# Kernel tuning notes

Measured on AMD Instinct MI355X. Metric: run time of the kernel, lower is better.

The kernel has to match this reference:

```python
import jax, jax.numpy as jnp
from jax import lax
import numpy as np

B, T, H, V, C = 64, 64, 1024, 32000, 10
Z, CD = 32, 8  # latent dim, cond embedding dim


def lstm_scan(x_tbh, h0, c0, Wih, Whh, bih, bhh):
    """PyTorch-convention LSTM over time. x_tbh: [T,B,H]; returns hs [T,B,H]."""
    def step(carry, x):
        h, c = carry
        gates = x @ Wih.T + bih + h @ Whh.T + bhh  # [B,4H]
        i, f, g, o = jnp.split(gates, 4, axis=-1)
        c = jax.nn.sigmoid(f) * c + jax.nn.sigmoid(i) * jnp.tanh(g)
        h = jax.nn.sigmoid(o) * jnp.tanh(c)
        return (h, c), h
    _, hs = lax.scan(step, (h0, c0), x_tbh)
    return hs


def setup_inputs() -> dict:
    key = jax.random.key(0)
    ks = jax.random.split(key, 24)
    s = 0.02
    d = {
        'input_word': jax.random.randint(ks[0], (B, T), 0, V),
        'cond': jax.random.randint(ks[1], (B,), 0, C),
        'emb_N': jax.random.normal(ks[2], (V, H), jnp.float32) * s,
        'Wih_N': jax.random.normal(ks[3], (4 * H, H), jnp.float32) * s,
        'Whh_N': jax.random.normal(ks[4], (4 * H, H), jnp.float32) * s,
        'bih_N': jnp.zeros((4 * H,), jnp.float32),
        'bhh_N': jnp.zeros((4 * H,), jnp.float32),
        'emb_D': jax.random.normal(ks[5], (V, H), jnp.float32) * s,
        'Wih_D': jax.random.normal(ks[6], (4 * H, H), jnp.float32) * s,
        'Whh_D': jax.random.normal(ks[7], (4 * H, H), jnp.float32) * s,
        'bih_D': jnp.zeros((4 * H,), jnp.float32),
        'bhh_D': jnp.zeros((4 * H,), jnp.float32),
        'emb_cond': jax.random.normal(ks[8], (C, CD), jnp.float32) * s,
        'W_mean': jax.random.normal(ks[9], (Z, H), jnp.float32) * s,
        'b_mean': jnp.zeros((Z,), jnp.float32),
        'W_logvar': jax.random.normal(ks[10], (Z, H), jnp.float32) * s,
        'b_logvar': jnp.zeros((Z,), jnp.float32),
        'W_st': jax.random.normal(ks[11], (H, Z + CD), jnp.float32) * s,
        'b_st': jnp.zeros((H,), jnp.float32),
        'W_out': jax.random.normal(ks[12], (V, H), jnp.float32) * s,
        'b_out': jnp.zeros((V,), jnp.float32),
        'eps': jax.random.normal(ks[13], (B, Z), jnp.float32),
    }
    return d


def reference(input_word, cond, emb_N, Wih_N, Whh_N, bih_N, bhh_N,
              emb_D, Wih_D, Whh_D, bih_D, bhh_D, emb_cond,
              W_mean, b_mean, W_logvar, b_logvar, W_st, b_st,
              W_out, b_out, eps):
    cond_e = emb_cond[cond]                              # [B,8]
    # ---- encoder ----
    x_enc = jnp.transpose(emb_N[input_word], (1, 0, 2))  # [T,B,H]
    h0 = jnp.concatenate([jnp.zeros((B, H - CD), x_enc.dtype), cond_e], axis=-1)
    c0 = jnp.zeros((B, H), x_enc.dtype)
    hs = lstm_scan(x_enc, h0, c0, Wih_N, Whh_N, bih_N, bhh_N)
    h_t = hs[-1]                                         # [B,H]
    mean_h = h_t @ W_mean.T + b_mean                     # [B,32]
    logvar_h = h_t @ W_logvar.T + b_logvar               # [B,32]
    latent_h = eps * jnp.exp(0.5 * logvar_h) + mean_h    # reparameterize
    # ---- decoder (teacher forcing, start token 0) ----
    hd0 = jnp.concatenate([latent_h, cond_e], axis=-1) @ W_st.T + b_st  # [B,H]
    cd0 = jnp.zeros((B, H), hd0.dtype)
    dec_tok = jnp.concatenate(
        [jnp.zeros((B, 1), input_word.dtype), input_word[:, :-1]], axis=1)
    x_dec = jnp.transpose(emb_D[dec_tok], (1, 0, 2))     # [T,B,H]
    hs_d = lstm_scan(x_dec, hd0, cd0, Wih_D, Whh_D, bih_D, bhh_D)  # [T,B,H]
    logits = hs_d @ W_out.T + b_out                      # [T,B,V]
    return jnp.transpose(logits, (1, 0, 2))              # [B,T,V]
```

## Files before the change

kernel.cpp:

```cpp
#include <hip/hip_runtime.h>
#include <hip/hip_bf16.h>

typedef unsigned short u16;
typedef unsigned int   u32;
typedef unsigned long long u64;
typedef __attribute__((ext_vector_type(8))) short short8;
typedef __attribute__((ext_vector_type(4))) float f32x4;

#define DEVINL static __device__ __forceinline__

DEVINL u16 f2bf(float x) {
  u32 u = __float_as_uint(x);
  u32 r = (u + 0x7fffu + ((u >> 16) & 1u)) >> 16;
  return (u16)r;
}

#define GLD16(gp, lp) __builtin_amdgcn_global_load_lds(                     \
    (const __attribute__((address_space(1))) u32*)(gp),                     \
    (__attribute__((address_space(3))) u32*)(lp), 16, 0, 0)

__global__ __launch_bounds__(256) void conv_all(
    const float* __restrict__ s0, u16* __restrict__ d0,
    const float* __restrict__ s1, u16* __restrict__ d1,
    const float* __restrict__ s2, u16* __restrict__ d2,
    const float* __restrict__ s3, u16* __restrict__ d3,
    const float* __restrict__ s4, u16* __restrict__ d4) {
  const float* s; u16* d; int local;
  int blk = blockIdx.x;
  if (blk < 16384) {
    int p = blk >> 12; local = blk & 4095;
    s = (p == 0) ? s0 : (p == 1) ? s1 : (p == 2) ? s2 : s3;
    d = (p == 0) ? d0 : (p == 1) ? d1 : (p == 2) ? d2 : d3;
  } else {
    s = s4; d = d4; local = blk - 16384;
  }
  int i = local * 256 + threadIdx.x;
  float4 v = ((const float4*)s)[i];
  ushort4 o;
  o.x = f2bf(v.x); o.y = f2bf(v.y); o.z = f2bf(v.z); o.w = f2bf(v.w);
  ((ushort4*)d)[i] = o;
}

__global__ __launch_bounds__(256) void prep_small(
    const int* __restrict__ cond, const float* __restrict__ emb_cond,
    const float* __restrict__ bihN, const float* __restrict__ bhhN,
    const float* __restrict__ bihD, const float* __restrict__ bhhD,
    float* __restrict__ ce, float* __restrict__ biasN, float* __restrict__ biasD,
    u32* __restrict__ bar) {
  int tid = blockIdx.x * 256 + threadIdx.x;
  if (tid < 512) {
    int b = tid >> 3, j = tid & 7;
    ce[tid] = emb_cond[cond[b] * 8 + j];
  }
  int i = tid - 512;
  if (i >= 0 && i < 4096) {
    biasN[i] = bihN[i] + bhhN[i];
    biasD[i] = bihD[i] + bhhD[i];
  }
  int k = tid - 4608;
  if (k >= 0 && k < 512) bar[k] = 0;
}

__global__ __launch_bounds__(256) void init_enc(const float* __restrict__ ce,
                                                u16* __restrict__ hb0) {
  int tid = blockIdx.x * 256 + threadIdx.x;
  int b = tid >> 10, col = tid & 1023;
  float v = (col >= 1016) ? ce[b * 8 + (col - 1016)] : 0.f;
  hb0[tid] = f2bf(v);
}

__global__ __launch_bounds__(256) void gather_kernel(const float* __restrict__ emb,
                                                     const int* __restrict__ words,
                                                     u16* __restrict__ X, int dec) {
  int r = blockIdx.x;
  int t = r >> 6, b = r & 63;
  int tok = dec ? ((t == 0) ? 0 : words[b * 64 + t - 1]) : words[b * 64 + t];
  float4 v = ((const float4*)(emb + (size_t)tok * 1024))[threadIdx.x];
  ushort4 o;
  o.x = f2bf(v.x); o.y = f2bf(v.y); o.z = f2bf(v.z); o.w = f2bf(v.w);
  ((ushort4*)(X + (size_t)r * 1024))[threadIdx.x] = o;
}

template <int MODE>
__global__ __launch_bounds__(512) void gemm_bt_kernel(
    const u16* __restrict__ A, const u16* __restrict__ B,
    float* __restrict__ C, const float* __restrict__ bias, int N, int K) {
  __shared__ u16 lA[2][256 * 32];
  __shared__ u16 lB[2][128 * 32];
  const int tid = threadIdx.x;
  const int lane = tid & 63;
  const int wid = tid >> 6;

  int tile_m, tile_n;
  if (MODE == 0) {
    const int nn = N >> 7;
    const int nwg = gridDim.x;
    const int orig = blockIdx.x;
    const int wgid = (orig & 7) * (nwg >> 3) + (orig >> 3);
    tile_m = (wgid / nn) * 256;
    tile_n = (wgid % nn) * 128;
  } else {
    const int i = blockIdx.x;
    const int x = i & 7;
    const int k = i >> 3;
    const int mg = k >> 6;
    const int r  = k & 63;
    const int kn = r >> 1;
    const int mi = r & 1;
    const int tn = kn * 8 + x;
    if (tn >= 250) return;
    tile_m = (mg * 2 + mi) * 256;
    tile_n = tn * 128;
  }
  const int wm = wid >> 1, wn = wid & 1;

  const int ldr = lane >> 2;
  const int lko = (lane & 3) * 8;
  const int l15 = lane & 15;
  const int g4 = lane >> 4;

  const size_t aBase = (size_t)tile_m * K;
  const size_t bBase = (size_t)tile_n * K;

  auto stage = [&](int buf, int k0) {
#pragma unroll
    for (int q = 0; q < 2; ++q) {
      int chk = wid * 2 + q;
      int row = chk * 16 + ldr;
      GLD16(A + aBase + (size_t)row * K + k0 + lko, &lA[buf][chk * 512]);
    }
    int row = wid * 16 + ldr;
    GLD16(B + bBase + (size_t)row * K + k0 + lko, &lB[buf][wid * 512]);
  };

  f32x4 acc[4][4];
#pragma unroll
  for (int i = 0; i < 4; ++i)
#pragma unroll
    for (int j = 0; j < 4; ++j) acc[i][j] = (f32x4)0.f;

  stage(0, 0);
  __syncthreads();

  const int NIT = K >> 5;
  for (int it = 0; it < NIT; ++it) {
    const int cur = it & 1;
    if (it + 1 < NIT) stage(cur ^ 1, (it + 1) * 32);
    short8 af[4], bf[4];
#pragma unroll
    for (int i = 0; i < 4; ++i)
      af[i] = *(const short8*)&lA[cur][(wm * 64 + i * 16 + l15) * 32 + g4 * 8];
#pragma unroll
    for (int j = 0; j < 4; ++j)
      bf[j] = *(const short8*)&lB[cur][(wn * 64 + j * 16 + l15) * 32 + g4 * 8];
#pragma unroll
    for (int i = 0; i < 4; ++i)
#pragma unroll
      for (int j = 0; j < 4; ++j)
        acc[i][j] = __builtin_amdgcn_mfma_f32_16x16x32_bf16(af[i], bf[j], acc[i][j], 0, 0, 0);
    __syncthreads();
  }

#pragma unroll
  for (int i = 0; i < 4; ++i) {
    int row0 = tile_m + wm * 64 + i * 16 + (g4 << 2);
#pragma unroll
    for (int j = 0; j < 4; ++j) {
      int col = tile_n + wn * 64 + j * 16 + l15;
      float bv = bias[col];
#pragma unroll
      for (int e = 0; e < 4; ++e) {
        size_t o = (size_t)(row0 + e) * (size_t)N + col;
        float v = acc[i][j][e] + bv;
        if (MODE == 1) __builtin_nontemporal_store(v, &C[o]);
        else           C[o] = v;
      }
    }
  }
}

__global__ __launch_bounds__(512, 1) void lstm_cluster(
    const u16* __restrict__ Whh, const float* __restrict__ Xp,
    u16* __restrict__ hbuf,
    u16* __restrict__ hs_out,
    float* __restrict__ hT_out,
    u32* arrive) {
  __shared__ __align__(16) char smemA[32768];
  __shared__ float lg[8][16][16];
  const int tid = threadIdx.x;
  const int lane = tid & 63;
  const int v = tid >> 6;
  const int gate = v >> 1;
  const int ch = v & 1;
  const int wgi = blockIdx.x;
  const int c = wgi >> 5;
  const int j = wgi & 31;
  const int b0 = c * 16, col0 = j * 32;
  const int l15 = lane & 15, g4 = lane >> 4;

  short8 breg[32];
  {
    const u16* Brow = Whh + (size_t)(gate * 1024 + col0 + ch * 16 + l15) * 1024
                          + g4 * 8;
#pragma unroll
    for (int kk = 0; kk < 32; ++kk)
      breg[kk] = *(const short8*)(Brow + kk * 32);
  }

  const int crow = tid >> 5, colw = tid & 31;
  const int bg = b0 + crow, cgl = col0 + colw;
  const int ch2 = colw >> 4, cw = colw & 15;
  float creg = 0.f;

  for (int t = 0; t < 64; ++t) {
    const char* rbase = (const char*)(hbuf + (size_t)(t & 1) * 65536)
                      + (size_t)b0 * 2048;
    u32* wb32 = (u32*)(hbuf + (size_t)((t + 1) & 1) * 65536);

    size_t xrow = (size_t)(t * 64 + bg) * 4096 + cgl;
    float xg0 = __builtin_nontemporal_load(&Xp[xrow]);
    float xg1 = __builtin_nontemporal_load(&Xp[xrow + 1024]);
    float xg2 = __builtin_nontemporal_load(&Xp[xrow + 2048]);
    float xg3 = __builtin_nontemporal_load(&Xp[xrow + 3072]);

#pragma unroll
    for (int q = 0; q < 4; ++q) {
      int g = q * 512 + tid;
      int row = g >> 7;
      int cb = (g & 127) * 16;
      const u64* src = (const u64*)(rbase + (size_t)row * 2048 + cb);
      u64 lo = __hip_atomic_load(src,     __ATOMIC_RELAXED, __HIP_MEMORY_SCOPE_AGENT);
      u64 hi = __hip_atomic_load(src + 1, __ATOMIC_RELAXED, __HIP_MEMORY_SCOPE_AGENT);
      u64* d = (u64*)(smemA + row * 2048 + (cb ^ ((row & 7) << 4)));
      d[0] = lo; d[1] = hi;
    }
    __syncthreads();

    f32x4 a4[4] = {(f32x4)0.f, (f32x4)0.f, (f32x4)0.f, (f32x4)0.f};
#pragma unroll
    for (int kk = 0; kk < 32; ++kk) {
      int cb2 = kk * 64 + g4 * 16;
      const short8 a = *(const short8*)(smemA + l15 * 2048 + (cb2 ^ ((l15 & 7) << 4)));
      a4[kk & 3] = __builtin_amdgcn_mfma_f32_16x16x32_bf16(a, breg[kk], a4[kk & 3], 0, 0, 0);
    }
    f32x4 asum = a4[0] + a4[1] + a4[2] + a4[3];
    {
      int m = g4 * 4;
#pragma unroll
      for (int e = 0; e < 4; ++e) lg[v][m + e][l15] = asum[e];
    }
    __syncthreads();

    {
      float gi = lg[0 + ch2][crow][cw] + xg0;
      float gf = lg[2 + ch2][crow][cw] + xg1;
      float gg = lg[4 + ch2][crow][cw] + xg2;
      float go = lg[6 + ch2][crow][cw] + xg3;
      float si = 1.f / (1.f + __expf(-gi));
      float sf = 1.f / (1.f + __expf(-gf));
      float so = 1.f / (1.f + __expf(-go));
      float tg = tanhf(gg);
      float cn = sf * creg + si * tg;
      float hn = so * tanhf(cn);
      creg = cn;
      u16 h16 = f2bf(hn);
      u32 mine = h16;
      u32 other = (u32)__shfl_xor((int)mine, 1);
      if (!(colw & 1)) {
        u32 pk = mine | (other << 16);
        __hip_atomic_store(wb32 + (((size_t)bg * 1024 + cgl) >> 1), pk,
                           __ATOMIC_RELAXED, __HIP_MEMORY_SCOPE_AGENT);
      }
      if (hs_out) hs_out[((size_t)bg * 64 + t) * 1024 + cgl] = h16;
      if (hT_out && t == 63) hT_out[bg * 1024 + cgl] = hn;
    }

    if (t != 63) {
      u32 want = (u32)(t + 1);
      asm volatile("s_waitcnt vmcnt(0)" ::: "memory");
      __syncthreads();
      if (tid == 0)
        __hip_atomic_store(&arrive[wgi], want, __ATOMIC_RELAXED,
                           __HIP_MEMORY_SCOPE_AGENT);
      if (tid < 32) {
        int guard = 0;
        while (__hip_atomic_load(&arrive[c * 32 + tid], __ATOMIC_RELAXED,
                                 __HIP_MEMORY_SCOPE_AGENT) < want) {
          __builtin_amdgcn_s_sleep(2);
          if (++guard > (1 << 20)) break;
        }
      }
      __syncthreads();
    }
  }
}

__global__ __launch_bounds__(256) void latent_hd0_kernel(
    const float* hT, const float* Wm, const float* bm,
    const float* Wl, const float* bl, const float* Wst, const float* bst,
    const float* eps, const float* ce, u16* hb0) {
  __shared__ float red[64][4];
  __shared__ float ml[64];
  __shared__ float lat[40];
  int b = blockIdx.x;
  int tid = threadIdx.x;
  int o = tid >> 2, p = tid & 3;
  const float* w = (o < 32) ? (Wm + (size_t)o * 1024) : (Wl + (size_t)(o - 32) * 1024);
  const float* h = hT + (size_t)b * 1024;
  float s = 0.f;
  for (int k = p * 256; k < p * 256 + 256; ++k) s += h[k] * w[k];
  red[o][p] = s;
  __syncthreads();
  if (tid < 64) {
    float v = red[tid][0] + red[tid][1] + red[tid][2] + red[tid][3];
    v += (tid < 32) ? bm[tid] : bl[tid - 32];
    ml[tid] = v;
  }
  __syncthreads();
  if (tid < 32) lat[tid] = eps[b * 32 + tid] * __expf(0.5f * ml[32 + tid]) + ml[tid];
  if (tid >= 32 && tid < 40) lat[tid] = ce[b * 8 + (tid - 32)];
  __syncthreads();
  for (int hc = tid; hc < 1024; hc += 256) {
    float s2 = bst[hc];
    const float* wr = Wst + (size_t)hc * 40;
#pragma unroll
    for (int j = 0; j < 40; ++j) s2 += lat[j] * wr[j];
    hb0[b * 1024 + hc] = f2bf(s2);
  }
}

extern "C" void kernel_launch(void* const* d_in, const int* in_sizes, int n_in,
                              void* d_out, int out_size, void* d_ws, size_t ws_size,
                              hipStream_t stream) {
  const int*   input_word = (const int*)d_in[0];
  const int*   cond       = (const int*)d_in[1];
  const float* emb_N      = (const float*)d_in[2];
  const float* Wih_N      = (const float*)d_in[3];
  const float* Whh_N      = (const float*)d_in[4];
  const float* bih_N      = (const float*)d_in[5];
  const float* bhh_N      = (const float*)d_in[6];
  const float* emb_D      = (const float*)d_in[7];
  const float* Wih_D      = (const float*)d_in[8];
  const float* Whh_D      = (const float*)d_in[9];
  const float* bih_D      = (const float*)d_in[10];
  const float* bhh_D      = (const float*)d_in[11];
  const float* emb_cond   = (const float*)d_in[12];
  const float* W_mean     = (const float*)d_in[13];
  const float* b_mean     = (const float*)d_in[14];
  const float* W_logvar   = (const float*)d_in[15];
  const float* b_logvar   = (const float*)d_in[16];
  const float* W_st       = (const float*)d_in[17];
  const float* b_st       = (const float*)d_in[18];
  const float* W_out      = (const float*)d_in[19];
  const float* b_out      = (const float*)d_in[20];
  const float* eps        = (const float*)d_in[21];
  float* out = (float*)d_out;

  char* ws = (char*)d_ws;
  size_t off = 0;
  auto alloc = [&](size_t b) { size_t p = off; off += (b + 255) & ~(size_t)255; return p; };
  u16*   wihN = (u16*)(ws + alloc(4096ull * 1024 * 2));
  u16*   whhN = (u16*)(ws + alloc(4096ull * 1024 * 2));
  u16*   wihD = (u16*)(ws + alloc(4096ull * 1024 * 2));
  u16*   whhD = (u16*)(ws + alloc(4096ull * 1024 * 2));
  u16*   wout = (u16*)(ws + alloc(32000ull * 1024 * 2));
  u16*   Xe   = (u16*)(ws + alloc(4096ull * 1024 * 2));
  u16*   Xd   = (u16*)(ws + alloc(4096ull * 1024 * 2));
  float* Xp   = (float*)(ws + alloc(4096ull * 4096 * 4));
  u16*   hsd  = (u16*)(ws + alloc(4096ull * 1024 * 2));
  u16*   hb   = (u16*)(ws + alloc(2ull * 64 * 1024 * 2));
  float* hf   = (float*)(ws + alloc(64ull * 1024 * 4));
  float* biasN = (float*)(ws + alloc(4096 * 4));
  float* biasD = (float*)(ws + alloc(4096 * 4));
  float* ce    = (float*)(ws + alloc(64 * 8 * 4));
  u32*   bar   = (u32*)(ws + alloc(2048));
  if (off > ws_size) return;

  conv_all<<<48384, 256, 0, stream>>>(Wih_N, wihN, Whh_N, whhN,
                                      Wih_D, wihD, Whh_D, whhD, W_out, wout);
  prep_small<<<20, 256, 0, stream>>>(cond, emb_cond, bih_N, bhh_N, bih_D, bhh_D,
                                     ce, biasN, biasD, bar);
  gather_kernel<<<4096, 256, 0, stream>>>(emb_N, input_word, Xe, 0);
  gather_kernel<<<4096, 256, 0, stream>>>(emb_D, input_word, Xd, 1);
  init_enc<<<256, 256, 0, stream>>>(ce, hb);

  gemm_bt_kernel<0><<<512, 512, 0, stream>>>(Xe, wihN, Xp, biasN, 4096, 1024);
  lstm_cluster<<<128, 512, 0, stream>>>(whhN, Xp, hb, nullptr, hf, bar + 0);
  latent_hd0_kernel<<<64, 256, 0, stream>>>(hf, W_mean, b_mean, W_logvar, b_logvar,
                                            W_st, b_st, eps, ce, hb);
  gemm_bt_kernel<0><<<512, 512, 0, stream>>>(Xd, wihD, Xp, biasD, 4096, 1024);
  lstm_cluster<<<128, 512, 0, stream>>>(whhD, Xp, hb, hsd, nullptr, bar + 256);
  gemm_bt_kernel<1><<<4096, 512, 0, stream>>>(hsd, wout, out, b_out, 32000, 1024);
}
```

Baseline: 1.066 ms.

## Overlap decoder input GEMM with encoder LSTM in one fused launch

```diff
diff --git a/kernel.cpp b/kernel.cpp
--- a/kernel.cpp
+++ b/kernel.cpp
@@ -81,37 +81,20 @@
   ((ushort4*)(X + (size_t)r * 1024))[threadIdx.x] = o;
 }
 
-template <int MODE>
-__global__ __launch_bounds__(512) void gemm_bt_kernel(
-    const u16* __restrict__ A, const u16* __restrict__ B,
-    float* __restrict__ C, const float* __restrict__ bias, int N, int K) {
-  __shared__ u16 lA[2][256 * 32];
-  __shared__ u16 lB[2][128 * 32];
+DEVINL void gemm0_body(char* smemc, int bid, int nwg,
+                       const u16* __restrict__ A, const u16* __restrict__ B,
+                       float* __restrict__ C, const float* __restrict__ bias,
+                       int N, int K) {
+  u16 (*lA)[256 * 32] = (u16(*)[256 * 32])smemc;
+  u16 (*lB)[128 * 32] = (u16(*)[128 * 32])(smemc + 32768);
   const int tid = threadIdx.x;
   const int lane = tid & 63;
   const int wid = tid >> 6;
 
-  int tile_m, tile_n;
-  if (MODE == 0) {
-    const int nn = N >> 7;
-    const int nwg = gridDim.x;
-    const int orig = blockIdx.x;
-    const int wgid = (orig & 7) * (nwg >> 3) + (orig >> 3);
-    tile_m = (wgid / nn) * 256;
-    tile_n = (wgid % nn) * 128;
-  } else {
-    const int i = blockIdx.x;
-    const int x = i & 7;
-    const int k = i >> 3;
-    const int mg = k >> 6;
-    const int r  = k & 63;
-    const int kn = r >> 1;
-    const int mi = r & 1;
-    const int tn = kn * 8 + x;
-    if (tn >= 250) return;
-    tile_m = (mg * 2 + mi) * 256;
-    tile_n = tn * 128;
-  }
+  const int nn = N >> 7;
+  const int wgid = (bid & 7) * (nwg >> 3) + (bid >> 3);
+  const int tile_m = (wgid / nn) * 256;
+  const int tile_n = (wgid % nn) * 128;
   const int wm = wid >> 1, wn = wid & 1;
 
   const int ldr = lane >> 2;
@@ -169,30 +152,23 @@
       int col = tile_n + wn * 64 + j * 16 + l15;
       float bv = bias[col];
 #pragma unroll
-      for (int e = 0; e < 4; ++e) {
-        size_t o = (size_t)(row0 + e) * (size_t)N + col;
-        float v = acc[i][j][e] + bv;
-        if (MODE == 1) __builtin_nontemporal_store(v, &C[o]);
-        else           C[o] = v;
-      }
-    }
-  }
-}
-
-__global__ __launch_bounds__(512, 1) void lstm_cluster(
-    const u16* __restrict__ Whh, const float* __restrict__ Xp,
-    u16* __restrict__ hbuf,
-    u16* __restrict__ hs_out,
-    float* __restrict__ hT_out,
-    u32* arrive) {
-  __shared__ __align__(16) char smemA[32768];
-  __shared__ float lg[8][16][16];
+      for (int e = 0; e < 4; ++e)
+        C[(size_t)(row0 + e) * (size_t)N + col] = acc[i][j][e] + bv;
+    }
+  }
+}
+
+DEVINL void lstm_body(char* smemc, const u16* __restrict__ Whh,
+                      const float* __restrict__ Xp, u16* __restrict__ hbuf,
+                      u16* __restrict__ hs_out, float* __restrict__ hT_out,
+                      u32* arrive, int wgi) {
+  char* smemA = smemc;
+  float (*lg)[16][16] = (float(*)[16][16])(smemc + 32768);
   const int tid = threadIdx.x;
   const int lane = tid & 63;
   const int v = tid >> 6;
   const int gate = v >> 1;
   const int ch = v & 1;
-  const int wgi = blockIdx.x;
   const int c = wgi >> 5;
   const int j = wgi & 31;
   const int b0 = c * 16, col0 = j * 32;
@@ -212,16 +188,19 @@
   const int ch2 = colw >> 4, cw = colw & 15;
   float creg = 0.f;
 
+  float xg0, xg1, xg2, xg3;
+  {
+    size_t xrow = (size_t)bg * 4096 + cgl;
+    xg0 = __builtin_nontemporal_load(&Xp[xrow]);
+    xg1 = __builtin_nontemporal_load(&Xp[xrow + 1024]);
+    xg2 = __builtin_nontemporal_load(&Xp[xrow + 2048]);
+    xg3 = __builtin_nontemporal_load(&Xp[xrow + 3072]);
+  }
+
   for (int t = 0; t < 64; ++t) {
     const char* rbase = (const char*)(hbuf + (size_t)(t & 1) * 65536)
                       + (size_t)b0 * 2048;
     u32* wb32 = (u32*)(hbuf + (size_t)((t + 1) & 1) * 65536);
-
-    size_t xrow = (size_t)(t * 64 + bg) * 4096 + cgl;
-    float xg0 = __builtin_nontemporal_load(&Xp[xrow]);
-    float xg1 = __builtin_nontemporal_load(&Xp[xrow + 1024]);
-    float xg2 = __builtin_nontemporal_load(&Xp[xrow + 2048]);
-    float xg3 = __builtin_nontemporal_load(&Xp[xrow + 3072]);
 
 #pragma unroll
     for (int q = 0; q < 4; ++q) {
@@ -276,6 +255,13 @@
     }
 
     if (t != 63) {
+      {
+        size_t xrow = (size_t)((t + 1) * 64 + bg) * 4096 + cgl;
+        xg0 = __builtin_nontemporal_load(&Xp[xrow]);
+        xg1 = __builtin_nontemporal_load(&Xp[xrow + 1024]);
+        xg2 = __builtin_nontemporal_load(&Xp[xrow + 2048]);
+        xg3 = __builtin_nontemporal_load(&Xp[xrow + 3072]);
+      }
       u32 want = (u32)(t + 1);
       asm volatile("s_waitcnt vmcnt(0)" ::: "memory");
       __syncthreads();
@@ -291,6 +277,118 @@
         }
       }
       __syncthreads();
+    }
+  }
+}
+
+__global__ __launch_bounds__(512, 1) void lstm_cluster(
+    const u16* __restrict__ Whh, const float* __restrict__ Xp,
+    u16* __restrict__ hbuf, u16* __restrict__ hs_out,
+    float* __restrict__ hT_out, u32* arrive) {
+  __shared__ __align__(16) char smem[40960];
+  lstm_body(smem, Whh, Xp, hbuf, hs_out, hT_out, arrive, blockIdx.x);
+}
+
+__global__ __launch_bounds__(512) void gemm_bt0(
+    const u16* __restrict__ A, const u16* __restrict__ B,
+    float* __restrict__ C, const float* __restrict__ bias, int N, int K) {
+  __shared__ __align__(16) char smem[49152];
+  gemm0_body(smem, blockIdx.x, gridDim.x, A, B, C, bias, N, K);
+}
+
+__global__ __launch_bounds__(512, 1) void enc_fused(
+    const u16* __restrict__ whhN, const float* __restrict__ XpE,
+    u16* __restrict__ hbuf, float* __restrict__ hT_out, u32* arrive,
+    const u16* __restrict__ Xd, const u16* __restrict__ wihD,
+    float* __restrict__ XpD, const float* __restrict__ biasD) {
+  __shared__ __align__(16) char smem[49152];
+  if (blockIdx.x < 128)
+    lstm_body(smem, whhN, XpE, hbuf, nullptr, hT_out, arrive, blockIdx.x);
+  else
+    gemm0_body(smem, blockIdx.x - 128, 512, Xd, wihD, XpD, biasD, 4096, 1024);
+}
+
+__global__ __launch_bounds__(512) void gemm_bt1(
+    const u16* __restrict__ A, const u16* __restrict__ B,
+    float* __restrict__ C, const float* __restrict__ bias, int N, int K) {
+  __shared__ u16 lA[2][256 * 32];
+  __shared__ u16 lB[2][128 * 32];
+  const int tid = threadIdx.x;
+  const int lane = tid & 63;
+  const int wid = tid >> 6;
+
+  const int i = blockIdx.x;
+  const int x = i & 7;
+  const int k = i >> 3;
+  const int mg = k >> 6;
+  const int r  = k & 63;
+  const int kn = r >> 1;
+  const int mi = r & 1;
+  const int tn = kn * 8 + x;
+  if (tn >= 250) return;
+  const int tile_m = (mg * 2 + mi) * 256;
+  const int tile_n = tn * 128;
+  const int wm = wid >> 1, wn = wid & 1;
+
+  const int ldr = lane >> 2;
+  const int lko = (lane & 3) * 8;
+  const int l15 = lane & 15;
+  const int g4 = lane >> 4;
+
+  const size_t aBase = (size_t)tile_m * K;
+  const size_t bBase = (size_t)tile_n * K;
+
+  auto stage = [&](int buf, int k0) {
+#pragma unroll
+    for (int q = 0; q < 2; ++q) {
+      int chk = wid * 2 + q;
+      int row = chk * 16 + ldr;
+      GLD16(A + aBase + (size_t)row * K + k0 + lko, &lA[buf][chk * 512]);
+    }
+    int row = wid * 16 + ldr;
+    GLD16(B + bBase + (size_t)row * K + k0 + lko, &lB[buf][wid * 512]);
+  };
+
+  f32x4 acc[4][4];
+#pragma unroll
+  for (int i2 = 0; i2 < 4; ++i2)
+#pragma unroll
+    for (int j2 = 0; j2 < 4; ++j2) acc[i2][j2] = (f32x4)0.f;
+
+  stage(0, 0);
+  __syncthreads();
+
+  const int NIT = K >> 5;
+  for (int it = 0; it < NIT; ++it) {
+    const int cur = it & 1;
+    if (it + 1 < NIT) stage(cur ^ 1, (it + 1) * 32);
+    short8 af[4], bf[4];
+#pragma unroll
+    for (int i2 = 0; i2 < 4; ++i2)
+      af[i2] = *(const short8*)&lA[cur][(wm * 64 + i2 * 16 + l15) * 32 + g4 * 8];
+#pragma unroll
+    for (int j2 = 0; j2 < 4; ++j2)
+      bf[j2] = *(const short8*)&lB[cur][(wn * 64 + j2 * 16 + l15) * 32 + g4 * 8];
+#pragma unroll
+    for (int i2 = 0; i2 < 4; ++i2)
+#pragma unroll
+      for (int j2 = 0; j2 < 4; ++j2)
+        acc[i2][j2] = __builtin_amdgcn_mfma_f32_16x16x32_bf16(af[i2], bf[j2], acc[i2][j2], 0, 0, 0);
+    __syncthreads();
+  }
+
+#pragma unroll
+  for (int i2 = 0; i2 < 4; ++i2) {
+    int row0 = tile_m + wm * 64 + i2 * 16 + (g4 << 2);
+#pragma unroll
+    for (int j2 = 0; j2 < 4; ++j2) {
+      int col = tile_n + wn * 64 + j2 * 16 + l15;
+      float bv = bias[col];
+#pragma unroll
+      for (int e = 0; e < 4; ++e) {
+        size_t o = (size_t)(row0 + e) * (size_t)N + col;
+        __builtin_nontemporal_store(acc[i2][j2][e] + bv, &C[o]);
+      }
     }
   }
 }
@@ -374,7 +472,11 @@
   float* biasD = (float*)(ws + alloc(4096 * 4));
   float* ce    = (float*)(ws + alloc(64 * 8 * 4));
   u32*   bar   = (u32*)(ws + alloc(2048));
-  if (off > ws_size) return;
+  size_t base_off = off;
+  float* XpD2 = (float*)(ws + alloc(4096ull * 4096 * 4));
+  if (base_off > ws_size) return;
+  const bool fused = (off <= ws_size);
+  float* XpD = fused ? XpD2 : Xp;
 
   conv_all<<<48384, 256, 0, stream>>>(Wih_N, wihN, Whh_N, whhN,
                                       Wih_D, wihD, Whh_D, whhD, W_out, wout);
@@ -384,11 +486,17 @@
   gather_kernel<<<4096, 256, 0, stream>>>(emb_D, input_word, Xd, 1);
   init_enc<<<256, 256, 0, stream>>>(ce, hb);
 
-  gemm_bt_kernel<0><<<512, 512, 0, stream>>>(Xe, wihN, Xp, biasN, 4096, 1024);
-  lstm_cluster<<<128, 512, 0, stream>>>(whhN, Xp, hb, nullptr, hf, bar + 0);
+  gemm_bt0<<<512, 512, 0, stream>>>(Xe, wihN, Xp, biasN, 4096, 1024);
+  if (fused) {
+    enc_fused<<<640, 512, 0, stream>>>(whhN, Xp, hb, hf, bar + 0,
+                                       Xd, wihD, XpD, biasD);
+  } else {
+    lstm_cluster<<<128, 512, 0, stream>>>(whhN, Xp, hb, nullptr, hf, bar + 0);
+  }
   latent_hd0_kernel<<<64, 256, 0, stream>>>(hf, W_mean, b_mean, W_logvar, b_logvar,
                                             W_st, b_st, eps, ce, hb);
-  gemm_bt_kernel<0><<<512, 512, 0, stream>>>(Xd, wihD, Xp, biasD, 4096, 1024);
-  lstm_cluster<<<128, 512, 0, stream>>>(whhD, Xp, hb, hsd, nullptr, bar + 256);
-  gemm_bt_kernel<1><<<4096, 512, 0, stream>>>(hsd, wout, out, b_out, 32000, 1024);
-}
+  if (!fused)
+    gemm_bt0<<<512, 512, 0, stream>>>(Xd, wihD, XpD, biasD, 4096, 1024);
+  lstm_cluster<<<128, 512, 0, stream>>>(whhD, XpD, hb, hsd, nullptr, bar + 256);
+  gemm_bt1<<<4096, 512, 0, stream>>>(hsd, wout, out, b_out, 32000, 1024);
+}
```

Result: faster. 1.011 ms (-5.1%).
